# Optimization experiments

Measured on AMD Instinct MI355X. Metric: run time of the kernel, lower is better.

Reference implementation:

```python
import jax, jax.numpy as jnp
import numpy as np

MARGIN = 0.2  # from init_kwargs
N, D, N_CLASSES = 8192, 256, 64


def setup_inputs() -> dict:
    key = jax.random.key(0)
    k1, k2 = jax.random.split(key)
    embeddings = jax.random.normal(k1, (N, D), dtype=jnp.float32)
    targets = jax.random.randint(k2, (N,), 0, N_CLASSES, dtype=jnp.int64)
    return {"embeddings": embeddings, "targets": targets}


def _mine_triplets(embeddings, targets):
    sq = jnp.sum(embeddings * embeddings, axis=1)  # [N]
    dist = -2.0 * (embeddings @ embeddings.T) + sq[None, :] + sq[:, None]  # [N, N]
    pos_mask = targets[:, None] == targets[None, :]  # same label (incl. self, as in original)
    NEG_INF = jnp.asarray(-1e30, dist.dtype)
    POS_INF = jnp.asarray(1e30, dist.dtype)
    hardest_pos = jnp.argmax(jnp.where(pos_mask, dist, NEG_INF), axis=1)  # [N]
    hardest_neg = jnp.argmin(jnp.where(pos_mask, POS_INF, dist), axis=1)  # [N]
    anchors = jnp.arange(targets.shape[0])
    return jnp.stack([anchors, hardest_pos, hardest_neg], axis=1)  # [N, 3]


def reference(embeddings, targets):
    triplets = _mine_triplets(embeddings, targets)
    a, p, n = triplets[:, 0], triplets[:, 1], triplets[:, 2]
    ap = jnp.sum((embeddings[a] - embeddings[p]) ** 2, axis=1)
    an = jnp.sum((embeddings[a] - embeddings[n]) ** 2, axis=1)
    losses = jax.nn.relu(ap - an + MARGIN)
    return losses.mean(), triplets
```

## Files before the change

### kernel.cpp

```cpp
#include <hip/hip_runtime.h>
#include <hip/hip_bf16.h>

#define NROWS 8192
#define DDIM 256
#define MARGIN_F 0.2f

#define CSPLIT 8
#define NSTR 72

typedef _Float16 half8 __attribute__((ext_vector_type(8)));
typedef float f32x4 __attribute__((ext_vector_type(4)));
typedef int i32x4 __attribute__((ext_vector_type(4)));

__global__ __launch_bounds__(256)
void sq_kernel(const float* __restrict__ E, float* __restrict__ sq) {
  const int lane = threadIdx.x & 63;
  const int row = blockIdx.x * 4 + (threadIdx.x >> 6);
  const float4 v = *(const float4*)&E[row * DDIM + lane * 4];
  float s = v.x * v.x + v.y * v.y + v.z * v.z + v.w * v.w;
#pragma unroll
  for (int o = 32; o > 0; o >>= 1) s += __shfl_down(s, o, 64);
  if (lane == 0) sq[row] = s;
}

__device__ __forceinline__ void stage16(_Float16* S, const float* src) {
  const float4 f0 = *(const float4*)(src);
  const float4 f1 = *(const float4*)(src + 4);
  const float4 f2 = *(const float4*)(src + 8);
  const float4 f3 = *(const float4*)(src + 12);
  half8 H0, L0, H1, L1;
#define CVT(H, L, e, v) { _Float16 h = (_Float16)(v); H[e] = h; L[e] = (_Float16)((v) - (float)h); }
  CVT(H0, L0, 0, f0.x) CVT(H0, L0, 1, f0.y) CVT(H0, L0, 2, f0.z) CVT(H0, L0, 3, f0.w)
  CVT(H0, L0, 4, f1.x) CVT(H0, L0, 5, f1.y) CVT(H0, L0, 6, f1.z) CVT(H0, L0, 7, f1.w)
  CVT(H1, L1, 0, f2.x) CVT(H1, L1, 1, f2.y) CVT(H1, L1, 2, f2.z) CVT(H1, L1, 3, f2.w)
  CVT(H1, L1, 4, f3.x) CVT(H1, L1, 5, f3.y) CVT(H1, L1, 6, f3.z) CVT(H1, L1, 7, f3.w)
#undef CVT
  *(half8*)(S) = H0;
  *(half8*)(S + 8) = H1;
  *(half8*)(S + 32) = L0;
  *(half8*)(S + 40) = L1;
}

__global__ __launch_bounds__(256, 2)
void mine_kernel(const float* __restrict__ E, const int* __restrict__ T,
                 const float* __restrict__ sq,
                 float* __restrict__ pv, int* __restrict__ pi,
                 float* __restrict__ nv, int* __restrict__ ni) {
  __shared__ __align__(16) _Float16 Si[128 * NSTR];
  __shared__ __align__(16) _Float16 Sj[128 * NSTR];

  const int tid = threadIdx.x;
  const int lane = tid & 63;
  const int w = tid >> 6;
  const int wi = w & 1, wj = w >> 1;
  const int l15 = lane & 15, grp = lane >> 4;
  const int rowbase = blockIdx.y * 128;
  const int colbase0 = blockIdx.x * 1024;

  const int sr = tid >> 1;
  const int skq = (tid & 1) * 16;

  float sqi[4]; int ti[4];
#pragma unroll
  for (int fi = 0; fi < 4; ++fi) {
    const int i = rowbase + wi * 64 + fi * 16 + l15;
    sqi[fi] = sq[i];
    ti[fi] = T[i];
  }

  float bpv[4], bnv[4]; int bpi[4], bni[4];
#pragma unroll
  for (int fi = 0; fi < 4; ++fi) { bpv[fi] = -3e38f; bnv[fi] = 3e38f; bpi[fi] = 0; bni[fi] = 0; }

  for (int ct = 0; ct < 8; ++ct) {
    const int cb = colbase0 + ct * 128;
    f32x4 acc[4][4];
#pragma unroll
    for (int jf = 0; jf < 4; ++jf)
#pragma unroll
      for (int fi = 0; fi < 4; ++fi) acc[jf][fi] = (f32x4){0.f, 0.f, 0.f, 0.f};

    for (int kb = 0; kb < DDIM; kb += 32) {
      __syncthreads();
      stage16(&Si[sr * NSTR + skq], &E[(rowbase + sr) * DDIM + kb + skq]);
      stage16(&Sj[sr * NSTR + skq], &E[(cb + sr) * DDIM + kb + skq]);
      __syncthreads();

      half8 ajh[4], ajl[4];
#pragma unroll
      for (int jf = 0; jf < 4; ++jf) {
        const int o = (wj * 64 + jf * 16 + l15) * NSTR + grp * 8;
        ajh[jf] = *(const half8*)&Sj[o];
        ajl[jf] = *(const half8*)&Sj[o + 32];
      }
#pragma unroll
      for (int fi = 0; fi < 4; ++fi) {
        const int o = (wi * 64 + fi * 16 + l15) * NSTR + grp * 8;
        const half8 bh = *(const half8*)&Si[o];
        const half8 bl = *(const half8*)&Si[o + 32];
#pragma unroll
        for (int jf = 0; jf < 4; ++jf)
          acc[jf][fi] = __builtin_amdgcn_mfma_f32_16x16x32_f16(ajh[jf], bh, acc[jf][fi], 0, 0, 0);
#pragma unroll
        for (int jf = 0; jf < 4; ++jf)
          acc[jf][fi] = __builtin_amdgcn_mfma_f32_16x16x32_f16(ajl[jf], bh, acc[jf][fi], 0, 0, 0);
#pragma unroll
        for (int jf = 0; jf < 4; ++jf)
          acc[jf][fi] = __builtin_amdgcn_mfma_f32_16x16x32_f16(ajh[jf], bl, acc[jf][fi], 0, 0, 0);
      }
    }

#pragma unroll
    for (int jf = 0; jf < 4; ++jf) {
      const int jb = cb + wj * 64 + jf * 16 + grp * 4;
      const f32x4 sqj = *(const f32x4*)&sq[jb];
      const i32x4 tj = *(const i32x4*)&T[jb];
#pragma unroll
      for (int fi = 0; fi < 4; ++fi) {
#pragma unroll
        for (int r = 0; r < 4; ++r) {
          const float dst = fmaf(-2.f, acc[jf][fi][r], sqi[fi] + sqj[r]);
          const int jidx = jb + r;
          if (ti[fi] == tj[r]) {
            if (dst > bpv[fi]) { bpv[fi] = dst; bpi[fi] = jidx; }
          } else {
            if (dst < bnv[fi]) { bnv[fi] = dst; bni[fi] = jidx; }
          }
        }
      }
    }
  }

#pragma unroll
  for (int fi = 0; fi < 4; ++fi) {
#pragma unroll
    for (int off = 16; off <= 32; off <<= 1) {
      const float ov = __shfl_xor(bpv[fi], off, 64);
      const int oi = __shfl_xor(bpi[fi], off, 64);
      if (ov > bpv[fi] || (ov == bpv[fi] && oi < bpi[fi])) { bpv[fi] = ov; bpi[fi] = oi; }
      const float on = __shfl_xor(bnv[fi], off, 64);
      const int oni = __shfl_xor(bni[fi], off, 64);
      if (on < bnv[fi] || (on == bnv[fi] && oni < bni[fi])) { bnv[fi] = on; bni[fi] = oni; }
    }
  }

  __syncthreads();
  float4* scr = (float4*)Si;
  if (wj == 1 && lane < 16) {
#pragma unroll
    for (int fi = 0; fi < 4; ++fi)
      scr[wi * 64 + fi * 16 + lane] =
          make_float4(bpv[fi], __int_as_float(bpi[fi]), bnv[fi], __int_as_float(bni[fi]));
  }
  __syncthreads();
  if (wj == 0 && lane < 16) {
#pragma unroll
    for (int fi = 0; fi < 4; ++fi) {
      const float4 o = scr[wi * 64 + fi * 16 + lane];
      const int oi = __float_as_int(o.y), oni = __float_as_int(o.w);
      if (o.x > bpv[fi] || (o.x == bpv[fi] && oi < bpi[fi])) { bpv[fi] = o.x; bpi[fi] = oi; }
      if (o.z < bnv[fi] || (o.z == bnv[fi] && oni < bni[fi])) { bnv[fi] = o.z; bni[fi] = oni; }
      const int row = rowbase + wi * 64 + fi * 16 + lane;
      const int oidx = row * CSPLIT + blockIdx.x;
      pv[oidx] = bpv[fi]; pi[oidx] = bpi[fi]; nv[oidx] = bnv[fi]; ni[oidx] = bni[fi];
    }
  }
}

__global__ __launch_bounds__(256)
void finish_kernel(const float* __restrict__ E,
                   const float* __restrict__ pv, const int* __restrict__ pi,
                   const float* __restrict__ nv, const int* __restrict__ ni,
                   float* __restrict__ out, float* __restrict__ bl) {
  const int w = threadIdx.x >> 6, lane = threadIdx.x & 63;
  const int row = blockIdx.x * 4 + w;
  float Pv = -3e38f, Nv = 3e38f; int Pi = 0, Ni = 0;
#pragma unroll
  for (int s = 0; s < CSPLIT; ++s) {
    const float p = pv[row * CSPLIT + s]; const int px = pi[row * CSPLIT + s];
    if (p > Pv || (p == Pv && px < Pi)) { Pv = p; Pi = px; }
    const float n = nv[row * CSPLIT + s]; const int nx = ni[row * CSPLIT + s];
    if (n < Nv || (n == Nv && nx < Ni)) { Nv = n; Ni = nx; }
  }
  const float4 a = *(const float4*)&E[row * DDIM + lane * 4];
  const float4 p4 = *(const float4*)&E[Pi * DDIM + lane * 4];
  const float4 n4 = *(const float4*)&E[Ni * DDIM + lane * 4];
  float ap = (a.x - p4.x) * (a.x - p4.x) + (a.y - p4.y) * (a.y - p4.y)
           + (a.z - p4.z) * (a.z - p4.z) + (a.w - p4.w) * (a.w - p4.w);
  float an = (a.x - n4.x) * (a.x - n4.x) + (a.y - n4.y) * (a.y - n4.y)
           + (a.z - n4.z) * (a.z - n4.z) + (a.w - n4.w) * (a.w - n4.w);
#pragma unroll
  for (int o = 32; o > 0; o >>= 1) {
    ap += __shfl_down(ap, o, 64);
    an += __shfl_down(an, o, 64);
  }
  __shared__ float ls[4];
  if (lane == 0) {
    out[1 + row * 3 + 0] = (float)row;
    out[1 + row * 3 + 1] = (float)Pi;
    out[1 + row * 3 + 2] = (float)Ni;
    ls[w] = fmaxf(ap - an + MARGIN_F, 0.f);
  }
  __syncthreads();
  if (threadIdx.x == 0) bl[blockIdx.x] = (ls[0] + ls[1]) + (ls[2] + ls[3]);
}

__global__ __launch_bounds__(256)
void sum_kernel(const float* __restrict__ bl, float* __restrict__ out) {
  __shared__ float s[256];
  float t = 0.f;
#pragma unroll
  for (int r = 0; r < (NROWS / 4) / 256; ++r) t += bl[threadIdx.x + r * 256];
  s[threadIdx.x] = t;
  __syncthreads();
  for (int o = 128; o > 0; o >>= 1) {
    if (threadIdx.x < o) s[threadIdx.x] += s[threadIdx.x + o];
    __syncthreads();
  }
  if (threadIdx.x == 0) out[0] = s[0] * (1.f / NROWS);
}

extern "C" void kernel_launch(void* const* d_in, const int* in_sizes, int n_in,
                              void* d_out, int out_size, void* d_ws, size_t ws_size,
                              hipStream_t stream) {
  const float* E = (const float*)d_in[0];
  const int* T = (const int*)d_in[1];
  float* out = (float*)d_out;

  float* sq = (float*)d_ws;
  float* pv = sq + NROWS;
  int*   pi = (int*)(pv + NROWS * CSPLIT);
  float* nv = (float*)(pi + NROWS * CSPLIT);
  int*   ni = (int*)(nv + NROWS * CSPLIT);
  float* bl = (float*)(ni + NROWS * CSPLIT);

  sq_kernel<<<NROWS / 4, 256, 0, stream>>>(E, sq);
  mine_kernel<<<dim3(CSPLIT, NROWS / 128), 256, 0, stream>>>(E, T, sq, pv, pi, nv, ni);
  finish_kernel<<<NROWS / 4, 256, 0, stream>>>(E, pv, pi, nv, ni, out, bl);
  sum_kernel<<<1, 256, 0, stream>>>(bl, out);
}
```

Measured before the change: 165.7 us.

## Precompute fp16 hi/lo split in MFMA-tiled layout and double-buffer via global_load_lds

A prep kernel now converts the embeddings once into fp16 high and low parts, stored in a tile layout that matches the MFMA fragments, and computes the squared norms in the same pass. The mining kernel then streams these tiles straight into LDS with direct global-to-LDS loads, double-buffered across k-steps with one barrier per step. This removes the repeated fp32-to-fp16 split done by every block and the two-barrier staging loop, and lets memory loads overlap the MFMA work. In exchange it needs extra workspace, an extra write and read of the fp16 arrays, and twice the LDS, which may limit occupancy.

```diff
diff --git a/kernel.cpp b/kernel.cpp
--- a/kernel.cpp
+++ b/kernel.cpp
@@ -1,53 +1,62 @@
 #include <hip/hip_runtime.h>
-#include <hip/hip_bf16.h>
 
 #define NROWS 8192
 #define DDIM 256
 #define MARGIN_F 0.2f
-
 #define CSPLIT 8
-#define NSTR 72
 
 typedef _Float16 half8 __attribute__((ext_vector_type(8)));
 typedef float f32x4 __attribute__((ext_vector_type(4)));
 typedef int i32x4 __attribute__((ext_vector_type(4)));
 
+__device__ __forceinline__ void gld16(const void* g, void* l) {
+  __builtin_amdgcn_global_load_lds(
+      (const __attribute__((address_space(1))) void*)g,
+      (__attribute__((address_space(3))) void*)l, 16, 0, 0);
+}
+
 __global__ __launch_bounds__(256)
-void sq_kernel(const float* __restrict__ E, float* __restrict__ sq) {
-  const int lane = threadIdx.x & 63;
-  const int row = blockIdx.x * 4 + (threadIdx.x >> 6);
-  const float4 v = *(const float4*)&E[row * DDIM + lane * 4];
-  float s = v.x * v.x + v.y * v.y + v.z * v.z + v.w * v.w;
-#pragma unroll
-  for (int o = 32; o > 0; o >>= 1) s += __shfl_down(s, o, 64);
-  if (lane == 0) sq[row] = s;
-}
-
-__device__ __forceinline__ void stage16(_Float16* S, const float* src) {
-  const float4 f0 = *(const float4*)(src);
-  const float4 f1 = *(const float4*)(src + 4);
-  const float4 f2 = *(const float4*)(src + 8);
-  const float4 f3 = *(const float4*)(src + 12);
-  half8 H0, L0, H1, L1;
-#define CVT(H, L, e, v) { _Float16 h = (_Float16)(v); H[e] = h; L[e] = (_Float16)((v) - (float)h); }
-  CVT(H0, L0, 0, f0.x) CVT(H0, L0, 1, f0.y) CVT(H0, L0, 2, f0.z) CVT(H0, L0, 3, f0.w)
-  CVT(H0, L0, 4, f1.x) CVT(H0, L0, 5, f1.y) CVT(H0, L0, 6, f1.z) CVT(H0, L0, 7, f1.w)
-  CVT(H1, L1, 0, f2.x) CVT(H1, L1, 1, f2.y) CVT(H1, L1, 2, f2.z) CVT(H1, L1, 3, f2.w)
-  CVT(H1, L1, 4, f3.x) CVT(H1, L1, 5, f3.y) CVT(H1, L1, 6, f3.z) CVT(H1, L1, 7, f3.w)
-#undef CVT
-  *(half8*)(S) = H0;
-  *(half8*)(S + 8) = H1;
-  *(half8*)(S + 32) = L0;
-  *(half8*)(S + 40) = L1;
+void prep_kernel(const float* __restrict__ E, _Float16* __restrict__ Eh,
+                 _Float16* __restrict__ El, float* __restrict__ sq) {
+  const int t = threadIdx.x;
+  const int r = t >> 4;
+  const int cs = t & 15;
+  const int rg = blockIdx.x;
+  const int row = rg * 16 + r;
+  const float* src = &E[row * DDIM + cs * 16];
+  float s = 0.f;
+  half8 H[2], L[2];
+#pragma unroll
+  for (int h = 0; h < 2; ++h) {
+    const float4 f0 = *(const float4*)(src + h * 8);
+    const float4 f1 = *(const float4*)(src + h * 8 + 4);
+    const float v[8] = {f0.x, f0.y, f0.z, f0.w, f1.x, f1.y, f1.z, f1.w};
+#pragma unroll
+    for (int e = 0; e < 8; ++e) {
+      s = fmaf(v[e], v[e], s);
+      const _Float16 hi = (_Float16)v[e];
+      H[h][e] = hi;
+      L[h][e] = (_Float16)(v[e] - (float)hi);
+    }
+  }
+  const int kt = cs >> 1;
+  const int g0 = (cs & 1) * 2;
+  const int base = (rg * 8 + kt) * 512;
+  *(half8*)&Eh[base + g0 * 128 + r * 8] = H[0];
+  *(half8*)&Eh[base + (g0 + 1) * 128 + r * 8] = H[1];
+  *(half8*)&El[base + g0 * 128 + r * 8] = L[0];
+  *(half8*)&El[base + (g0 + 1) * 128 + r * 8] = L[1];
+#pragma unroll
+  for (int o = 8; o > 0; o >>= 1) s += __shfl_down(s, o, 16);
+  if (cs == 0) sq[row] = s;
 }
 
 __global__ __launch_bounds__(256, 2)
-void mine_kernel(const float* __restrict__ E, const int* __restrict__ T,
-                 const float* __restrict__ sq,
+void mine_kernel(const _Float16* __restrict__ Eh, const _Float16* __restrict__ El,
+                 const int* __restrict__ T, const float* __restrict__ sq,
                  float* __restrict__ pv, int* __restrict__ pi,
                  float* __restrict__ nv, int* __restrict__ ni) {
-  __shared__ __align__(16) _Float16 Si[128 * NSTR];
-  __shared__ __align__(16) _Float16 Sj[128 * NSTR];
+  __shared__ __align__(16) _Float16 S[2][4][4096];
 
   const int tid = threadIdx.x;
   const int lane = tid & 63;
@@ -57,8 +66,8 @@
   const int rowbase = blockIdx.y * 128;
   const int colbase0 = blockIdx.x * 1024;
 
-  const int sr = tid >> 1;
-  const int skq = (tid & 1) * 16;
+  const _Float16* srcArr = (w == 0 || w == 2) ? Eh : El;
+  const bool isRowSide = (w < 2);
 
   float sqi[4]; int ti[4];
 #pragma unroll
@@ -74,30 +83,37 @@
 
   for (int ct = 0; ct < 8; ++ct) {
     const int cb = colbase0 + ct * 128;
+    const int rb16 = (isRowSide ? rowbase : cb) >> 4;
+
     f32x4 acc[4][4];
 #pragma unroll
     for (int jf = 0; jf < 4; ++jf)
 #pragma unroll
       for (int fi = 0; fi < 4; ++fi) acc[jf][fi] = (f32x4){0.f, 0.f, 0.f, 0.f};
 
-    for (int kb = 0; kb < DDIM; kb += 32) {
-      __syncthreads();
-      stage16(&Si[sr * NSTR + skq], &E[(rowbase + sr) * DDIM + kb + skq]);
-      stage16(&Sj[sr * NSTR + skq], &E[(cb + sr) * DDIM + kb + skq]);
-      __syncthreads();
-
+#pragma unroll
+    for (int rg = 0; rg < 8; ++rg)
+      gld16(srcArr + ((rb16 + rg) * 8 + 0) * 512 + lane * 8, &S[0][w][rg * 512]);
+    __syncthreads();
+
+    int cur = 0;
+    for (int kt = 0; kt < 8; ++kt) {
+      if (kt < 7) {
+#pragma unroll
+        for (int rg = 0; rg < 8; ++rg)
+          gld16(srcArr + ((rb16 + rg) * 8 + kt + 1) * 512 + lane * 8,
+                &S[cur ^ 1][w][rg * 512]);
+      }
       half8 ajh[4], ajl[4];
 #pragma unroll
       for (int jf = 0; jf < 4; ++jf) {
-        const int o = (wj * 64 + jf * 16 + l15) * NSTR + grp * 8;
-        ajh[jf] = *(const half8*)&Sj[o];
-        ajl[jf] = *(const half8*)&Sj[o + 32];
+        ajh[jf] = *(const half8*)&S[cur][2][(wj * 4 + jf) * 512 + lane * 8];
+        ajl[jf] = *(const half8*)&S[cur][3][(wj * 4 + jf) * 512 + lane * 8];
       }
 #pragma unroll
       for (int fi = 0; fi < 4; ++fi) {
-        const int o = (wi * 64 + fi * 16 + l15) * NSTR + grp * 8;
-        const half8 bh = *(const half8*)&Si[o];
-        const half8 bl = *(const half8*)&Si[o + 32];
+        const half8 bh = *(const half8*)&S[cur][0][(wi * 4 + fi) * 512 + lane * 8];
+        const half8 bl = *(const half8*)&S[cur][1][(wi * 4 + fi) * 512 + lane * 8];
 #pragma unroll
         for (int jf = 0; jf < 4; ++jf)
           acc[jf][fi] = __builtin_amdgcn_mfma_f32_16x16x32_f16(ajh[jf], bh, acc[jf][fi], 0, 0, 0);
@@ -108,6 +124,8 @@
         for (int jf = 0; jf < 4; ++jf)
           acc[jf][fi] = __builtin_amdgcn_mfma_f32_16x16x32_f16(ajh[jf], bl, acc[jf][fi], 0, 0, 0);
       }
+      __syncthreads();
+      cur ^= 1;
     }
 
 #pragma unroll
@@ -145,7 +163,7 @@
   }
 
   __syncthreads();
-  float4* scr = (float4*)Si;
+  float4* scr = (float4*)&S[0][0][0];
   if (wj == 1 && lane < 16) {
 #pragma unroll
     for (int fi = 0; fi < 4; ++fi)
@@ -227,15 +245,17 @@
   const int* T = (const int*)d_in[1];
   float* out = (float*)d_out;
 
-  float* sq = (float*)d_ws;
+  _Float16* Eh = (_Float16*)d_ws;
+  _Float16* El = Eh + NROWS * DDIM;
+  float* sq = (float*)(El + NROWS * DDIM);
   float* pv = sq + NROWS;
   int*   pi = (int*)(pv + NROWS * CSPLIT);
   float* nv = (float*)(pi + NROWS * CSPLIT);
   int*   ni = (int*)(nv + NROWS * CSPLIT);
   float* bl = (float*)(ni + NROWS * CSPLIT);
 
-  sq_kernel<<<NROWS / 4, 256, 0, stream>>>(E, sq);
-  mine_kernel<<<dim3(CSPLIT, NROWS / 128), 256, 0, stream>>>(E, T, sq, pv, pi, nv, ni);
+  prep_kernel<<<NROWS / 16, 256, 0, stream>>>(E, Eh, El, sq);
+  mine_kernel<<<dim3(CSPLIT, NROWS / 128), 256, 0, stream>>>(Eh, El, T, sq, pv, pi, nv, ni);
   finish_kernel<<<NROWS / 4, 256, 0, stream>>>(E, pv, pi, nv, ni, out, bl);
   sum_kernel<<<1, 256, 0, stream>>>(bl, out);
 }
```

Result: faster. 137.0 us (-17.3%).
